# Optimization experiments

Measured on AMD Instinct MI355X. Metric: run time of the kernel, lower is better.

Reference implementation:

```python
import jax, jax.numpy as jnp
import numpy as np

B, S, F, P, D, H, L, FF, R = 64, 4096, 8, 16, 512, 8, 6, 2048, 8
NP = (S - P) // P + 1  # 256 patches (stride == patch_length)
DK = D // H
LORA_SCALING = 16.0 / 8.0  # lora_alpha / lora_rank


def setup_inputs() -> dict:
    key = jax.random.key(0)
    ks = iter(jax.random.split(key, 40))
    def nrm(shape, s=0.02):
        return jax.random.normal(next(ks), shape, jnp.float32) * s
    inp = {
        "x": jax.random.normal(next(ks), (B, S, F), jnp.float32),
        "patch_w": nrm((P * F, D)), "patch_b": jnp.zeros((D,), jnp.float32),
        "patch_ln_w": jnp.ones((D,), jnp.float32), "patch_ln_b": jnp.zeros((D,), jnp.float32),
        "pos_enc": nrm((1, NP, D)),
        "ln1_w": jnp.ones((L, D), jnp.float32), "ln1_b": jnp.zeros((L, D), jnp.float32),
        "q_w": nrm((L, D, D)), "q_b": jnp.zeros((L, D), jnp.float32),
        "k_w": nrm((L, D, D)), "k_b": jnp.zeros((L, D), jnp.float32),
        "v_w": nrm((L, D, D)), "v_b": jnp.zeros((L, D), jnp.float32),
        "lq_down": nrm((L, D, R)), "lq_up": nrm((L, R, D)),
        "lk_down": nrm((L, D, R)), "lk_up": nrm((L, R, D)),
        "lv_down": nrm((L, D, R)), "lv_up": nrm((L, R, D)),
        "o_w": nrm((L, D, D)), "o_b": jnp.zeros((L, D), jnp.float32),
        "ln2_w": jnp.ones((L, D), jnp.float32), "ln2_b": jnp.zeros((L, D), jnp.float32),
        "ff1_w": nrm((L, D, FF)), "ff1_b": jnp.zeros((L, FF), jnp.float32),
        "ff2_w": nrm((L, FF, D)), "ff2_b": jnp.zeros((L, D), jnp.float32),
        "norm_w": jnp.ones((D,), jnp.float32), "norm_b": jnp.zeros((D,), jnp.float32),
    }
    return inp


def _layer_norm(x, w, b):
    m = jnp.mean(x, -1, keepdims=True)
    v = jnp.mean(jnp.square(x - m), -1, keepdims=True)
    return (x - m) * jax.lax.rsqrt(v + 1e-5) * w + b


def _forward(x, patch_w, patch_b, patch_ln_w, patch_ln_b, pos_enc,
             ln1_w, ln1_b, q_w, q_b, k_w, k_b, v_w, v_b,
             lq_down, lq_up, lk_down, lk_up, lv_down, lv_up,
             o_w, o_b, ln2_w, ln2_b, ff1_w, ff1_b, ff2_w, ff2_b,
             norm_w, norm_b):
    # Patch embedding: [B,S,F] -> [B,F,S] -> unfold(stride==patch) -> [B,NP,F*P]
    patches = x.transpose(0, 2, 1).reshape(B, F, NP, P).transpose(0, 2, 1, 3).reshape(B, NP, F * P)
    h = _layer_norm(patches @ patch_w + patch_b, patch_ln_w, patch_ln_b) + pos_enc
    inv_scale = 1.0 / np.sqrt(DK).astype(np.float32)
    for i in range(L):
        y = _layer_norm(h, ln1_w[i], ln1_b[i])
        q = y @ q_w[i] + q_b[i] + (y @ lq_down[i]) @ lq_up[i] * LORA_SCALING
        k = y @ k_w[i] + k_b[i] + (y @ lk_down[i]) @ lk_up[i] * LORA_SCALING
        v = y @ v_w[i] + v_b[i] + (y @ lv_down[i]) @ lv_up[i] * LORA_SCALING
        q = q.reshape(B, NP, H, DK)
        k = k.reshape(B, NP, H, DK)
        v = v.reshape(B, NP, H, DK)
        scores = jnp.einsum('bqhd,bkhd->bhqk', q, k) * inv_scale
        probs = jax.nn.softmax(scores, axis=-1)
        attn = jnp.einsum('bhqk,bkhd->bqhd', probs, v).reshape(B, NP, D)
        h = h + attn @ o_w[i] + o_b[i]
        y = _layer_norm(h, ln2_w[i], ln2_b[i])
        ff = jax.nn.gelu(y @ ff1_w[i] + ff1_b[i], approximate=False) @ ff2_w[i] + ff2_b[i]
        h = h + ff
    h = _layer_norm(h, norm_w, norm_b)
    return h.mean(axis=1)  # [B, D]


def reference(x, patch_w, patch_b, patch_ln_w, patch_ln_b, pos_enc,
              ln1_w, ln1_b, q_w, q_b, k_w, k_b, v_w, v_b,
              lq_down, lq_up, lk_down, lk_up, lv_down, lv_up,
              o_w, o_b, ln2_w, ln2_b, ff1_w, ff1_b, ff2_w, ff2_b,
              norm_w, norm_b):
    return _forward(x, patch_w, patch_b, patch_ln_w, patch_ln_b, pos_enc,
                    ln1_w, ln1_b, q_w, q_b, k_w, k_b, v_w, v_b,
                    lq_down, lq_up, lk_down, lk_up, lv_down, lv_up,
                    o_w, o_b, ln2_w, ln2_b, ff1_w, ff1_b, ff2_w, ff2_b,
                    norm_w, norm_b)
```

## Files before the change

kernel.cpp:

```cpp
#include <hip/hip_runtime.h>
#include <cstdint>
#include <cstddef>

constexpr int BATCH = 64, SEQ = 4096, FEAT = 8, PLEN = 16;
constexpr int DMODEL = 512, NHEAD = 8, NLAYER = 6, DFF = 2048;
constexpr int NPATCH = 256, MROWS = BATCH * NPATCH;
constexpr int DK = 64;
constexpr int LDSP = 72;

typedef unsigned short u16t;
typedef __bf16 bf16t;
typedef bf16t bf16x8 __attribute__((ext_vector_type(8)));
typedef short s16x4 __attribute__((ext_vector_type(4)));
typedef float f32x4 __attribute__((ext_vector_type(4)));

__device__ __forceinline__ float b2f(u16t u) {
  union { unsigned int ui; float f; } v; v.ui = ((unsigned int)u) << 16; return v.f;
}
__device__ __forceinline__ u16t f2b(float f) {
  union { float f; unsigned int ui; } v; v.f = f;
  return (u16t)((v.ui + 0x7fffu + ((v.ui >> 16) & 1u)) >> 16);
}
__device__ __forceinline__ void g2l16(void* lds, const void* g) {
  __builtin_amdgcn_global_load_lds(
      (__attribute__((address_space(1))) void*)g,
      (__attribute__((address_space(3))) void*)lds, 16, 0, 0);
}

__device__ __forceinline__ float gelu_erf(float x) {
  const float z = fabsf(x) * 0.70710678118654752f;
  const float t = __builtin_amdgcn_rcpf(__builtin_fmaf(0.3275911f, z, 1.0f));
  float p = __builtin_fmaf(1.061405429f, t, -1.453152027f);
  p = __builtin_fmaf(p, t, 1.421413741f);
  p = __builtin_fmaf(p, t, -0.284496736f);
  p = __builtin_fmaf(p, t, 0.254829592f);
  const float e = __expf(-z * z);
  const float er = __builtin_fmaf(-p * t, e, 1.0f);
  const float s = copysignf(er, x);
  return 0.5f * x * (1.0f + s);
}

__global__ __launch_bounds__(256, 2) void k_gemm(
    const u16t* __restrict__ A, const u16t* __restrict__ Bt,
    const float* __restrict__ bias, const float* __restrict__ b2,
    const float* __restrict__ b3, float* __restrict__ Cf,
    u16t* __restrict__ Cb, int M, int N, int K, int mode)
{
  __shared__ __align__(16) u16t SH[3 * 12288];

  const int nbn = N >> 7;
  const int cpx = gridDim.x >> 3;
  const int wgid = (blockIdx.x & 7) * cpx + (blockIdx.x >> 3);
  const int bm = (wgid / nbn) << 8;
  const int bn = (wgid % nbn) << 7;

  const int tid = threadIdx.x, wave = tid >> 6, lane = tid & 63;
  const int lr = lane & 15, quad = lane >> 4;
  const int wm = (wave >> 1) << 7;
  const int wn = (wave & 1) << 6;

  const int srow = lane >> 2;
  const int sseg = (lane & 3) ^ ((lane >> 3) & 3);
  const u16t* gA = A + (size_t)(bm + wave * 64 + srow) * K + sseg * 8;
  const u16t* gB = Bt + (size_t)(bn + wave * 32 + srow) * K + sseg * 8;
  const size_t r16K = (size_t)16 * K;

  const int sw8 = (quad ^ ((lr >> 1) & 3)) << 3;
  const int aoff = (wm + lr) * 32 + sw8;
  const int boff = 8192 + (wn + lr) * 32 + sw8;

  f32x4 acc[4][8] = {};

  u16t* buf0 = SH;
  u16t* buf1 = SH + 12288;
  u16t* buf2 = SH + 24576;

  #pragma unroll
  for (int j = 0; j < 4; ++j) g2l16(&buf0[(wave * 4 + j) * 512], gA + (size_t)j * r16K);
  #pragma unroll
  for (int j = 0; j < 2; ++j) g2l16(&buf0[8192 + (wave * 2 + j) * 512], gB + (size_t)j * r16K);
  gA += 32; gB += 32;
  #pragma unroll
  for (int j = 0; j < 4; ++j) g2l16(&buf1[(wave * 4 + j) * 512], gA + (size_t)j * r16K);
  #pragma unroll
  for (int j = 0; j < 2; ++j) g2l16(&buf1[8192 + (wave * 2 + j) * 512], gB + (size_t)j * r16K);
  gA += 32; gB += 32;

  const int nt = K >> 5;
  for (int t = 0; t < nt - 1; ++t) {
    asm volatile("s_waitcnt vmcnt(6)" ::: "memory");
    __builtin_amdgcn_s_barrier();
    asm volatile("" ::: "memory");
    if (t + 2 < nt) {
      #pragma unroll
      for (int j = 0; j < 4; ++j) g2l16(&buf2[(wave * 4 + j) * 512], gA + (size_t)j * r16K);
      #pragma unroll
      for (int j = 0; j < 2; ++j) g2l16(&buf2[8192 + (wave * 2 + j) * 512], gB + (size_t)j * r16K);
      gA += 32; gB += 32;
    }
    bf16x8 af[8], bfr[4];
    #pragma unroll
    for (int i = 0; i < 8; ++i) af[i] = *(const bf16x8*)&buf0[aoff + i * 512];
    #pragma unroll
    for (int j = 0; j < 4; ++j) bfr[j] = *(const bf16x8*)&buf0[boff + j * 512];
    __builtin_amdgcn_s_setprio(1);
    #pragma unroll
    for (int j = 0; j < 4; ++j)
      #pragma unroll
      for (int i = 0; i < 8; ++i)
        acc[j][i] = __builtin_amdgcn_mfma_f32_16x16x32_bf16(bfr[j], af[i], acc[j][i], 0, 0, 0);
    __builtin_amdgcn_s_setprio(0);
    u16t* tmp = buf0; buf0 = buf1; buf1 = buf2; buf2 = tmp;
  }
  {
    asm volatile("s_waitcnt vmcnt(0)" ::: "memory");
    __builtin_amdgcn_s_barrier();
    asm volatile("" ::: "memory");
    bf16x8 af[8], bfr[4];
    #pragma unroll
    for (int i = 0; i < 8; ++i) af[i] = *(const bf16x8*)&buf0[aoff + i * 512];
    #pragma unroll
    for (int j = 0; j < 4; ++j) bfr[j] = *(const bf16x8*)&buf0[boff + j * 512];
    __builtin_amdgcn_s_setprio(1);
    #pragma unroll
    for (int j = 0; j < 4; ++j)
      #pragma unroll
      for (int i = 0; i < 8; ++i)
        acc[j][i] = __builtin_amdgcn_mfma_f32_16x16x32_bf16(bfr[j], af[i], acc[j][i], 0, 0, 0);
    __builtin_amdgcn_s_setprio(0);
  }

  const float* bp = bias;
  int reg0 = 0;
  if (bias && b2) { reg0 = (bn >> 9) << 9; bp = reg0 == 0 ? bias : (reg0 == 512 ? b2 : b3); }
  float4 bv[4];
  #pragma unroll
  for (int jN = 0; jN < 4; ++jN) {
    const int gn0 = bn + wn + jN * 16 + quad * 4;
    bv[jN] = bias ? *(const float4*)&bp[gn0 - reg0] : make_float4(0.f, 0.f, 0.f, 0.f);
  }

  if (mode <= 1) {
    __syncthreads();
    u16t* E = SH;
    #pragma unroll
    for (int jN = 0; jN < 4; ++jN) {
      const int cl = wn + jN * 16 + quad * 4;
      const int seg = cl >> 3, intra = cl & 7;
      #pragma unroll
      for (int iM = 0; iM < 8; ++iM) {
        const int r = wm + iM * 16 + lr;
        float v0 = acc[jN][iM][0] + bv[jN].x, v1 = acc[jN][iM][1] + bv[jN].y;
        float v2 = acc[jN][iM][2] + bv[jN].z, v3 = acc[jN][iM][3] + bv[jN].w;
        union { u16t h[4]; uint2 u; } pk;
        if (mode == 1) {
          pk.h[0] = f2b(gelu_erf(v0)); pk.h[1] = f2b(gelu_erf(v1));
          pk.h[2] = f2b(gelu_erf(v2)); pk.h[3] = f2b(gelu_erf(v3));
        } else {
          pk.h[0] = f2b(v0); pk.h[1] = f2b(v1); pk.h[2] = f2b(v2); pk.h[3] = f2b(v3);
        }
        *(uint2*)&E[r * 128 + ((seg ^ (r & 7)) << 3) + intra] = pk.u;
      }
    }
    __syncthreads();
    const int rr = tid >> 2, s0 = tid & 3;
    #pragma unroll
    for (int pass = 0; pass < 4; ++pass) {
      const int r = pass * 64 + rr;
      u16t* gout = Cb + (size_t)(bm + r) * N + bn;
      #pragma unroll
      for (int it = 0; it < 4; ++it) {
        const int s = s0 + it * 4;
        uint4 u = *(const uint4*)&E[r * 128 + ((s ^ (r & 7)) << 3)];
        *(uint4*)(gout + s * 8) = u;
      }
    }
  } else {
    #pragma unroll
    for (int jN = 0; jN < 4; ++jN) {
      const int gn0 = bn + wn + jN * 16 + quad * 4;
      #pragma unroll
      for (int iM = 0; iM < 8; ++iM) {
        const int gm = bm + wm + iM * 16 + lr;
        const size_t off = (size_t)gm * N + gn0;
        float v0 = acc[jN][iM][0] + bv[jN].x, v1 = acc[jN][iM][1] + bv[jN].y;
        float v2 = acc[jN][iM][2] + bv[jN].z, v3 = acc[jN][iM][3] + bv[jN].w;
        if (mode == 2) {
          float4 c = *(float4*)(Cf + off);
          c.x += v0; c.y += v1; c.z += v2; c.w += v3;
          *(float4*)(Cf + off) = c;
        } else {
          *(float4*)(Cf + off) = make_float4(v0, v1, v2, v3);
        }
      }
    }
  }
}

__global__ __launch_bounds__(256) void k_prep_w(
    const float* __restrict__ W, const float* __restrict__ down,
    const float* __restrict__ up, u16t* __restrict__ Wt, int K, int N,
    size_t ostride, int orow0)
{
  __shared__ float t[32][33];
  const int z = blockIdx.z;
  const float* Wz = W + (size_t)z * K * N;
  u16t* Wtz = Wt + (size_t)z * ostride + (size_t)orow0 * K;
  const int k0 = blockIdx.x * 32, n0 = blockIdx.y * 32;
  const int tx = threadIdx.x & 31, ty = threadIdx.x >> 5;
  for (int i = ty; i < 32; i += 8) {
    const int kk = k0 + i, nn = n0 + tx;
    float v = Wz[(size_t)kk * N + nn];
    if (down) {
      const float* dz = down + (size_t)z * K * 8 + (size_t)kk * 8;
      const float* uz = up + (size_t)z * 8 * N + nn;
      float lv = 0.f;
      #pragma unroll
      for (int r = 0; r < 8; ++r) lv += dz[r] * uz[(size_t)r * N];
      v += 2.0f * lv;
    }
    t[i][tx] = v;
  }
  __syncthreads();
  for (int i = ty; i < 32; i += 8)
    Wtz[(size_t)(n0 + i) * K + k0 + tx] = f2b(t[tx][i]);
}

__global__ void k_patch(const float* __restrict__ x, u16t* __restrict__ pt) {
  const int idx = blockIdx.x * 256 + threadIdx.x;
  const int col = idx & 127, row = idx >> 7;
  const int f = col >> 4, pp = col & 15;
  const int b = row >> 8, np = row & 255;
  pt[idx] = f2b(x[(((size_t)b << 12) + np * 16 + pp) * 8 + f]);
}

__global__ __launch_bounds__(256) void k_ln(
    const float* __restrict__ xin, const float* __restrict__ w,
    const float* __restrict__ bb, u16t* __restrict__ y)
{
  const int row = blockIdx.x * 4 + (threadIdx.x >> 6);
  const int lane = threadIdx.x & 63;
  const float4* xr = (const float4*)(xin + (size_t)row * 512);
  float4 a = xr[lane * 2], c = xr[lane * 2 + 1];
  float s = a.x + a.y + a.z + a.w + c.x + c.y + c.z + c.w;
  float qq = a.x * a.x + a.y * a.y + a.z * a.z + a.w * a.w +
             c.x * c.x + c.y * c.y + c.z * c.z + c.w * c.w;
  #pragma unroll
  for (int o = 32; o > 0; o >>= 1) { s += __shfl_xor(s, o); qq += __shfl_xor(qq, o); }
  const float mean = s * (1.f / 512.f);
  const float rs = rsqrtf(qq * (1.f / 512.f) - mean * mean + 1e-5f);
  const float4* wr = (const float4*)w; const float4* br = (const float4*)bb;
  float4 w0 = wr[lane * 2], w1 = wr[lane * 2 + 1];
  float4 b0 = br[lane * 2], b1 = br[lane * 2 + 1];
  union { u16t h[8]; uint4 v; } pk;
  pk.h[0] = f2b((a.x - mean) * rs * w0.x + b0.x);
  pk.h[1] = f2b((a.y - mean) * rs * w0.y + b0.y);
  pk.h[2] = f2b((a.z - mean) * rs * w0.z + b0.z);
  pk.h[3] = f2b((a.w - mean) * rs * w0.w + b0.w);
  pk.h[4] = f2b((c.x - mean) * rs * w1.x + b1.x);
  pk.h[5] = f2b((c.y - mean) * rs * w1.y + b1.y);
  pk.h[6] = f2b((c.z - mean) * rs * w1.z + b1.z);
  pk.h[7] = f2b((c.w - mean) * rs * w1.w + b1.w);
  *(uint4*)(y + (size_t)row * 512 + lane * 8) = pk.v;
}

__global__ __launch_bounds__(256) void k_ln_pos(
    const float* __restrict__ xin, const float* __restrict__ w,
    const float* __restrict__ bb, const float* __restrict__ pos,
    float* __restrict__ h)
{
  const int row = blockIdx.x * 4 + (threadIdx.x >> 6);
  const int lane = threadIdx.x & 63;
  const float4* xr = (const float4*)(xin + (size_t)row * 512);
  float4 a = xr[lane * 2], c = xr[lane * 2 + 1];
  float s = a.x + a.y + a.z + a.w + c.x + c.y + c.z + c.w;
  float qq = a.x * a.x + a.y * a.y + a.z * a.z + a.w * a.w +
             c.x * c.x + c.y * c.y + c.z * c.z + c.w * c.w;
  #pragma unroll
  for (int o = 32; o > 0; o >>= 1) { s += __shfl_xor(s, o); qq += __shfl_xor(qq, o); }
  const float mean = s * (1.f / 512.f);
  const float rs = rsqrtf(qq * (1.f / 512.f) - mean * mean + 1e-5f);
  const float4* wr = (const float4*)w; const float4* br = (const float4*)bb;
  float4 w0 = wr[lane * 2], w1 = wr[lane * 2 + 1];
  float4 b0 = br[lane * 2], b1 = br[lane * 2 + 1];
  const int np = row & 255;
  const float4* pr = (const float4*)(pos + (size_t)np * 512);
  float4 p0 = pr[lane * 2], p1 = pr[lane * 2 + 1];
  float4 o0, o1;
  o0.x = (a.x - mean) * rs * w0.x + b0.x + p0.x;
  o0.y = (a.y - mean) * rs * w0.y + b0.y + p0.y;
  o0.z = (a.z - mean) * rs * w0.z + b0.z + p0.z;
  o0.w = (a.w - mean) * rs * w0.w + b0.w + p0.w;
  o1.x = (c.x - mean) * rs * w1.x + b1.x + p1.x;
  o1.y = (c.y - mean) * rs * w1.y + b1.y + p1.y;
  o1.z = (c.z - mean) * rs * w1.z + b1.z + p1.z;
  o1.w = (c.w - mean) * rs * w1.w + b1.w + p1.w;
  float4* hr = (float4*)(h + (size_t)row * 512);
  hr[lane * 2] = o0; hr[lane * 2 + 1] = o1;
}

__global__ __launch_bounds__(256) void k_attn(
    const u16t* __restrict__ qkv, u16t* __restrict__ out)
{
  __shared__ __align__(16) u16t Qs[128 * LDSP];
  __shared__ __align__(16) u16t Ks[64 * LDSP];
  __shared__ __align__(16) u16t Vts[64 * LDSP];

  const int bh = blockIdx.x >> 1, half = blockIdx.x & 1;
  const int b = bh >> 3, hd = bh & 7;
  const int tid = threadIdx.x, wave = tid >> 6, lane = tid & 63;
  const int lr = lane & 15, quad = lane >> 4;

  const size_t rowbase = (size_t)b * 256;
  const u16t* qg = qkv + (rowbase + half * 128) * 1536 + hd * 64;
  const u16t* kg = qkv + rowbase * 1536 + 512 + hd * 64;
  const u16t* vg = qkv + rowbase * 1536 + 1024 + hd * 64;

  #pragma unroll
  for (int i = 0; i < 4; ++i) {
    const int idx = tid + i * 256, row = idx >> 3, seg = idx & 7;
    uint4 u = *(const uint4*)(qg + (size_t)row * 1536 + seg * 8);
    *(uint4*)&Qs[row * LDSP + seg * 8] = u;
  }
  __syncthreads();

  bf16x8 qf[2][2];
  #pragma unroll
  for (int qi = 0; qi < 2; ++qi)
    #pragma unroll
    for (int dh = 0; dh < 2; ++dh)
      qf[qi][dh] = *(const bf16x8*)&Qs[(wave * 32 + qi * 16 + lr) * LDSP + dh * 32 + quad * 8];

  f32x4 O[2][4] = {};
  float mrun[2] = {-1e30f, -1e30f}, lrun[2] = {0.f, 0.f};

  for (int c = 0; c < 4; ++c) {
    __syncthreads();
    #pragma unroll
    for (int i = 0; i < 2; ++i) {
      const int idx = tid + i * 256, row = idx >> 3, seg = idx & 7;
      uint4 u = *(const uint4*)(kg + (size_t)(c * 64 + row) * 1536 + seg * 8);
      *(uint4*)&Ks[row * LDSP + seg * 8] = u;
    }
    {
      const int key = tid & 63, dg = (tid >> 6) * 16;
      const u16t* vrow = vg + (size_t)(c * 64 + key) * 1536 + dg;
      union { u16t h[16]; uint4 v[2]; } tmp;
      tmp.v[0] = *(const uint4*)(vrow);
      tmp.v[1] = *(const uint4*)(vrow + 8);
      #pragma unroll
      for (int i = 0; i < 16; ++i)
        Vts[(dg + i) * LDSP + key] = tmp.h[i];
    }
    __syncthreads();

    #pragma unroll
    for (int qi = 0; qi < 2; ++qi) {
      f32x4 s[4];
      #pragma unroll
      for (int kt = 0; kt < 4; ++kt) {
        f32x4 a = {};
        #pragma unroll
        for (int dh = 0; dh < 2; ++dh) {
          bf16x8 kf = *(const bf16x8*)&Ks[(kt * 16 + lr) * LDSP + dh * 32 + quad * 8];
          a = __builtin_amdgcn_mfma_f32_16x16x32_bf16(kf, qf[qi][dh], a, 0, 0, 0);
        }
        s[kt] = a;
      }
      constexpr float SC = 0.125f * 1.44269504088896f;
      float cmax = -1e30f;
      #pragma unroll
      for (int kt = 0; kt < 4; ++kt)
        #pragma unroll
        for (int r = 0; r < 4; ++r) { s[kt][r] *= SC; cmax = fmaxf(cmax, s[kt][r]); }
      cmax = fmaxf(cmax, __shfl_xor(cmax, 16));
      cmax = fmaxf(cmax, __shfl_xor(cmax, 32));
      const float mn = fmaxf(mrun[qi], cmax);
      const float alpha = exp2f(mrun[qi] - mn);
      mrun[qi] = mn;
      float lsum = 0.f;
      s16x4 pf[4];
      #pragma unroll
      for (int kt = 0; kt < 4; ++kt) {
        #pragma unroll
        for (int r = 0; r < 4; ++r) {
          const u16t eb = f2b(exp2f(s[kt][r] - mn));
          pf[kt][r] = (short)eb;
          lsum += b2f(eb);
        }
      }
      lsum += __shfl_xor(lsum, 16);
      lsum += __shfl_xor(lsum, 32);
      lrun[qi] = lrun[qi] * alpha + lsum;
      #pragma unroll
      for (int dt = 0; dt < 4; ++dt) {
        f32x4 o = O[qi][dt];
        o[0] *= alpha; o[1] *= alpha; o[2] *= alpha; o[3] *= alpha;
        #pragma unroll
        for (int kt = 0; kt < 4; ++kt) {
          s16x4 vf = *(const s16x4*)&Vts[(dt * 16 + lr) * LDSP + kt * 16 + quad * 4];
          o = __builtin_amdgcn_mfma_f32_16x16x16bf16_1k(vf, pf[kt], o, 0, 0, 0);
        }
        O[qi][dt] = o;
      }
    }
  }
  #pragma unroll
  for (int qi = 0; qi < 2; ++qi) {
    const float rl = 1.f / lrun[qi];
    u16t* orow = out + (rowbase + half * 128 + wave * 32 + qi * 16 + lr) * 512 + hd * 64 + quad * 4;
    #pragma unroll
    for (int dt = 0; dt < 4; ++dt) {
      union { u16t h[4]; uint2 v; } pk;
      #pragma unroll
      for (int r = 0; r < 4; ++r) pk.h[r] = f2b(O[qi][dt][r] * rl);
      *(uint2*)(orow + dt * 16) = pk.v;
    }
  }
}

__global__ void k_mean(const u16t* __restrict__ y, float* __restrict__ out) {
  const int b = blockIdx.x, d = threadIdx.x;
  float s = 0.f;
  #pragma unroll 8
  for (int np = 0; np < 256; ++np) s += b2f(y[((size_t)b * 256 + np) * 512 + d]);
  out[(size_t)b * 512 + d] = s * (1.f / 256.f);
}

extern "C" void kernel_launch(void* const* d_in, const int* in_sizes, int n_in,
                              void* d_out, int out_size, void* d_ws, size_t ws_size,
                              hipStream_t stream)
{
  (void)in_sizes; (void)n_in; (void)out_size;
  const float* x        = (const float*)d_in[0];
  const float* patch_w  = (const float*)d_in[1];
  const float* patch_b  = (const float*)d_in[2];
  const float* patch_ln_w = (const float*)d_in[3];
  const float* patch_ln_b = (const float*)d_in[4];
  const float* pos_enc  = (const float*)d_in[5];
  const float* ln1_w    = (const float*)d_in[6];
  const float* ln1_b    = (const float*)d_in[7];
  const float* q_w      = (const float*)d_in[8];
  const float* q_b      = (const float*)d_in[9];
  const float* k_w      = (const float*)d_in[10];
  const float* k_b      = (const float*)d_in[11];
  const float* v_w      = (const float*)d_in[12];
  const float* v_b      = (const float*)d_in[13];
  const float* lq_down  = (const float*)d_in[14];
  const float* lq_up    = (const float*)d_in[15];
  const float* lk_down  = (const float*)d_in[16];
  const float* lk_up    = (const float*)d_in[17];
  const float* lv_down  = (const float*)d_in[18];
  const float* lv_up    = (const float*)d_in[19];
  const float* o_w      = (const float*)d_in[20];
  const float* o_b      = (const float*)d_in[21];
  const float* ln2_w    = (const float*)d_in[22];
  const float* ln2_b    = (const float*)d_in[23];
  const float* ff1_w    = (const float*)d_in[24];
  const float* ff1_b    = (const float*)d_in[25];
  const float* ff2_w    = (const float*)d_in[26];
  const float* ff2_b    = (const float*)d_in[27];
  const float* norm_w   = (const float*)d_in[28];
  const float* norm_b   = (const float*)d_in[29];
  float* out = (float*)d_out;

  char* p = (char*)d_ws;
  float* h  = (float*)p;  p += (size_t)MROWS * 512 * 4;
  u16t*  y  = (u16t*)p;   p += (size_t)MROWS * 512 * 2;
  char* uni = p;          p += (size_t)4 * MROWS * 512 * 2;
  u16t* qkvb = (u16t*)uni;
  u16t* ab = (u16t*)(uni + (size_t)MROWS * 1536 * 2);
  u16t* g  = (u16t*)uni;
  float* pe = (float*)uni;
  u16t* pt = (u16t*)(uni + (size_t)MROWS * 512 * 4);
  u16t* wqkv = (u16t*)p; p += (size_t)NLAYER * 1536 * 512 * 2;
  u16t* wo = (u16t*)p; p += (size_t)NLAYER * 512 * 512 * 2;
  u16t* w1 = (u16t*)p; p += (size_t)NLAYER * 512 * 2048 * 2;
  u16t* w2 = (u16t*)p; p += (size_t)NLAYER * 2048 * 512 * 2;
  u16t* wp = (u16t*)p; p += (size_t)512 * 128 * 2;
  if ((size_t)(p - (char*)d_ws) > ws_size) return;

  const dim3 blk(256);
  const size_t QKVS = (size_t)1536 * 512;
  k_prep_w<<<dim3(16, 16, NLAYER), blk, 0, stream>>>(q_w, lq_down, lq_up, wqkv, 512, 512, QKVS, 0);
  k_prep_w<<<dim3(16, 16, NLAYER), blk, 0, stream>>>(k_w, lk_down, lk_up, wqkv, 512, 512, QKVS, 512);
  k_prep_w<<<dim3(16, 16, NLAYER), blk, 0, stream>>>(v_w, lv_down, lv_up, wqkv, 512, 512, QKVS, 1024);
  k_prep_w<<<dim3(16, 16, NLAYER), blk, 0, stream>>>(o_w, nullptr, nullptr, wo, 512, 512, (size_t)512 * 512, 0);
  k_prep_w<<<dim3(16, 64, NLAYER), blk, 0, stream>>>(ff1_w, nullptr, nullptr, w1, 512, 2048, (size_t)512 * 2048, 0);
  k_prep_w<<<dim3(64, 16, NLAYER), blk, 0, stream>>>(ff2_w, nullptr, nullptr, w2, 2048, 512, (size_t)2048 * 512, 0);
  k_prep_w<<<dim3(4, 16, 1),       blk, 0, stream>>>(patch_w, nullptr, nullptr, wp, 128, 512, 0, 0);

  k_patch<<<dim3(MROWS * 128 / 256), blk, 0, stream>>>(x, pt);
  k_gemm<<<dim3(64 * 4), blk, 0, stream>>>(pt, wp, patch_b, nullptr, nullptr, pe, nullptr, MROWS, 512, 128, 3);
  k_ln_pos<<<dim3(MROWS / 4), blk, 0, stream>>>(pe, patch_ln_w, patch_ln_b, pos_enc, h);

  for (int i = 0; i < NLAYER; ++i) {
    const size_t ws512 = (size_t)i * 512 * 512, wsff = (size_t)i * 512 * 2048;
    k_ln<<<dim3(MROWS / 4), blk, 0, stream>>>(h, ln1_w + i * 512, ln1_b + i * 512, y);
    k_gemm<<<dim3(64 * 12), blk, 0, stream>>>(y, wqkv + i * QKVS, q_b + i * 512, k_b + i * 512,
                                              v_b + i * 512, nullptr, qkvb, MROWS, 1536, 512, 0);
    k_attn<<<dim3(1024), blk, 0, stream>>>(qkvb, ab);
    k_gemm<<<dim3(64 * 4), blk, 0, stream>>>(ab, wo + ws512, o_b + i * 512, nullptr, nullptr, h, nullptr, MROWS, 512, 512, 2);
    k_ln<<<dim3(MROWS / 4), blk, 0, stream>>>(h, ln2_w + i * 512, ln2_b + i * 512, y);
    k_gemm<<<dim3(64 * 16), blk, 0, stream>>>(y, w1 + wsff, ff1_b + i * 2048, nullptr, nullptr, nullptr, g, MROWS, 2048, 512, 1);
    k_gemm<<<dim3(64 * 4), blk, 0, stream>>>(g, w2 + wsff, ff2_b + i * 512, nullptr, nullptr, h, nullptr, MROWS, 512, 2048, 2);
  }
  k_ln<<<dim3(MROWS / 4), blk, 0, stream>>>(h, norm_w, norm_b, y);
  k_mean<<<dim3(BATCH), dim3(512), 0, stream>>>(y, out);
}
```

Before: 1.501 ms.

## Add 256x256-tile 512-thread GEMM kernel for QKV and FF1 projections

Adds a new GEMM kernel with 256x256 output tiles, 8 waves, K-step 64 with double-buffered LDS staging, and fine-grained phases that interleave global-to-LDS loads with MFMA sub-blocks. It is used for the QKV and FF1 projections, which have bf16 outputs. The larger tile raises arithmetic intensity and cuts redundant global loads of A and B. It also changes the staging address pattern in the existing GEMM so that consecutive waves load interleaved 16-row chunks. The cost is 128 KB of LDS per block and fewer blocks in flight, so a poor schedule could leave MFMA units idle.

After: 1.600 ms. 1.07x slower.

```diff
diff --git a/kernel.cpp b/kernel.cpp
--- a/kernel.cpp
+++ b/kernel.cpp
@@ -59,11 +59,9 @@
   const int wm = (wave >> 1) << 7;
   const int wn = (wave & 1) << 6;
 
-  const int srow = lane >> 2;
   const int sseg = (lane & 3) ^ ((lane >> 3) & 3);
-  const u16t* gA = A + (size_t)(bm + wave * 64 + srow) * K + sseg * 8;
-  const u16t* gB = Bt + (size_t)(bn + wave * 32 + srow) * K + sseg * 8;
-  const size_t r16K = (size_t)16 * K;
+  const u16t* gA = A + (size_t)(bm + (lane >> 2)) * K + sseg * 8;
+  const u16t* gB = Bt + (size_t)(bn + (lane >> 2)) * K + sseg * 8;
 
   const int sw8 = (quad ^ ((lr >> 1) & 3)) << 3;
   const int aoff = (wm + lr) * 32 + sw8;
@@ -75,29 +73,24 @@
   u16t* buf1 = SH + 12288;
   u16t* buf2 = SH + 24576;
 
-  #pragma unroll
-  for (int j = 0; j < 4; ++j) g2l16(&buf0[(wave * 4 + j) * 512], gA + (size_t)j * r16K);
-  #pragma unroll
-  for (int j = 0; j < 2; ++j) g2l16(&buf0[8192 + (wave * 2 + j) * 512], gB + (size_t)j * r16K);
-  gA += 32; gB += 32;
-  #pragma unroll
-  for (int j = 0; j < 4; ++j) g2l16(&buf1[(wave * 4 + j) * 512], gA + (size_t)j * r16K);
-  #pragma unroll
-  for (int j = 0; j < 2; ++j) g2l16(&buf1[8192 + (wave * 2 + j) * 512], gB + (size_t)j * r16K);
-  gA += 32; gB += 32;
+#define STAGE_R10(BUF_, S_) do {                                               \
+    g2l16((BUF_) + wave * 512,        gA + (size_t)(wave * 16) * K + (S_) * 32);   \
+    g2l16((BUF_) + (wave + 4) * 512,  gA + (size_t)((wave + 4) * 16) * K + (S_) * 32); \
+    g2l16((BUF_) + (wave + 8) * 512,  gA + (size_t)((wave + 8) * 16) * K + (S_) * 32); \
+    g2l16((BUF_) + (wave + 12) * 512, gA + (size_t)((wave + 12) * 16) * K + (S_) * 32); \
+    g2l16((BUF_) + 8192 + wave * 512, gB + (size_t)(wave * 16) * K + (S_) * 32);   \
+    g2l16((BUF_) + 8192 + (wave + 4) * 512, gB + (size_t)((wave + 4) * 16) * K + (S_) * 32); \
+  } while (0)
 
   const int nt = K >> 5;
+  STAGE_R10(buf0, 0);
+  STAGE_R10(buf1, 1);
+
   for (int t = 0; t < nt - 1; ++t) {
     asm volatile("s_waitcnt vmcnt(6)" ::: "memory");
     __builtin_amdgcn_s_barrier();
     asm volatile("" ::: "memory");
-    if (t + 2 < nt) {
-      #pragma unroll
-      for (int j = 0; j < 4; ++j) g2l16(&buf2[(wave * 4 + j) * 512], gA + (size_t)j * r16K);
-      #pragma unroll
-      for (int j = 0; j < 2; ++j) g2l16(&buf2[8192 + (wave * 2 + j) * 512], gB + (size_t)j * r16K);
-      gA += 32; gB += 32;
-    }
+    if (t + 2 < nt) STAGE_R10(buf2, t + 2);
     bf16x8 af[8], bfr[4];
     #pragma unroll
     for (int i = 0; i < 8; ++i) af[i] = *(const bf16x8*)&buf0[aoff + i * 512];
@@ -129,6 +122,7 @@
         acc[j][i] = __builtin_amdgcn_mfma_f32_16x16x32_bf16(bfr[j], af[i], acc[j][i], 0, 0, 0);
     __builtin_amdgcn_s_setprio(0);
   }
+#undef STAGE_R10
 
   const float* bp = bias;
   int reg0 = 0;
@@ -194,6 +188,152 @@
         }
       }
     }
+  }
+}
+
+__global__ __launch_bounds__(512, 2) void k_gemm256(
+    const u16t* __restrict__ A, const u16t* __restrict__ Bt,
+    const float* __restrict__ bias, const float* __restrict__ b2,
+    const float* __restrict__ b3, u16t* __restrict__ Cb,
+    int M, int N, int K, int mode)
+{
+  __shared__ __align__(16) u16t SH[65536];
+
+  const int nbn = N >> 8;
+  const int cpx = gridDim.x >> 3;
+  const int wgid = (blockIdx.x & 7) * cpx + (blockIdx.x >> 3);
+  const int bm = (wgid / nbn) << 8;
+  const int bn = (wgid % nbn) << 8;
+
+  const int tid = threadIdx.x, wave = tid >> 6, lane = tid & 63;
+  const int lr = lane & 15, quad = lane >> 4, lr7 = lane & 7;
+  const int wm = (wave >> 2) << 7;
+  const int wn = (wave & 3) << 6;
+  const int hA = wave >> 2;
+  const int hB = (wave >> 1) & 1;
+  const int rB0 = (wave & 1) << 6;
+
+  const int srow = tid >> 3;
+  const int sdst = srow * 64 + (tid & 7) * 8;
+  const int ssegx = ((tid & 7) ^ (srow & 7)) * 8;
+  const u16t* gA0 = A + (size_t)(bm + srow) * K + ssegx;
+  const u16t* gB0 = Bt + (size_t)(bn + srow) * K + ssegx;
+
+  f32x4 acc[4][8] = {};
+  bf16x8 af_[4][2], bfr_[2][2];
+  const int NT = K >> 6, NIT = NT >> 1;
+
+#define STG(T_, H_) do { if ((T_) < NT) {                                      \
+    const int dd_ = ((T_) & 1) * 2;                                            \
+    u16t* dst_; const u16t* sp_;                                               \
+    if ((H_) < 2) {                                                            \
+      dst_ = SH + (dd_ + (H_)) * 8192 + sdst;                                  \
+      sp_ = gA0 + (size_t)((H_) * 128) * K + (T_) * 64;                        \
+    } else {                                                                   \
+      dst_ = SH + 32768 + (dd_ + (H_) - 2) * 8192 + sdst;                      \
+      sp_ = gB0 + (size_t)(((H_) - 2) * 128) * K + (T_) * 64;                  \
+    }                                                                          \
+    g2l16(dst_, sp_); g2l16(dst_ + 4096, sp_ + (size_t)64 * K);                \
+  } } while (0)
+
+#define GATE2 asm volatile("s_waitcnt vmcnt(2)" ::: "memory")
+#define GATE0 asm volatile("s_waitcnt vmcnt(0)" ::: "memory")
+#define GNONE (void)0
+
+#define PHASE(D_, MQ_, NQ_, ST_, SHF_, GATE_) do {                             \
+    if ((NQ_) == 0) {                                                          \
+      _Pragma("unroll") for (int i = 0; i < 4; ++i)                            \
+        _Pragma("unroll") for (int kk = 0; kk < 2; ++kk)                       \
+          af_[i][kk] = *(const bf16x8*)&SH[((D_) * 2 + hA) * 8192 +            \
+              (((MQ_) * 4 + i) * 16 + lr) * 64 + (((kk * 4 + quad) ^ lr7) << 3)]; \
+    }                                                                          \
+    _Pragma("unroll") for (int j = 0; j < 2; ++j)                              \
+      _Pragma("unroll") for (int kk = 0; kk < 2; ++kk)                         \
+        bfr_[j][kk] = *(const bf16x8*)&SH[32768 + ((D_) * 2 + hB) * 8192 +     \
+            (rB0 + ((NQ_) * 2 + j) * 16 + lr) * 64 + (((kk * 4 + quad) ^ lr7) << 3)]; \
+    STG(ST_, SHF_);                                                            \
+    if ((NQ_) == 0) asm volatile("s_waitcnt lgkmcnt(8)" ::: "memory");         \
+    __builtin_amdgcn_s_barrier();                                              \
+    asm volatile("s_waitcnt lgkmcnt(0)" ::: "memory");                         \
+    __builtin_amdgcn_sched_barrier(0);                                         \
+    __builtin_amdgcn_s_setprio(1);                                             \
+    _Pragma("unroll") for (int j = 0; j < 2; ++j)                              \
+      _Pragma("unroll") for (int i = 0; i < 4; ++i)                            \
+        _Pragma("unroll") for (int kk = 0; kk < 2; ++kk)                       \
+          acc[(NQ_) * 2 + j][(MQ_) * 4 + i] = __builtin_amdgcn_mfma_f32_16x16x32_bf16( \
+              bfr_[j][kk], af_[i][kk], acc[(NQ_) * 2 + j][(MQ_) * 4 + i], 0, 0, 0); \
+    __builtin_amdgcn_s_setprio(0);                                             \
+    GATE_;                                                                     \
+    __builtin_amdgcn_s_barrier();                                              \
+  } while (0)
+
+  STG(0, 0); STG(0, 1); STG(0, 2); STG(0, 3); STG(1, 0);
+  GATE2;
+  __builtin_amdgcn_s_barrier();
+
+  for (int i = 0; i < NIT - 1; ++i) {
+    const int tb = 2 * i;
+    PHASE(0, 0, 0, tb + 1, 1, GNONE);
+    PHASE(0, 0, 1, tb + 1, 2, GNONE);
+    PHASE(0, 1, 0, tb + 1, 3, GNONE);
+    PHASE(0, 1, 1, tb + 2, 0, GATE2);
+    PHASE(1, 0, 0, tb + 2, 1, GNONE);
+    PHASE(1, 0, 1, tb + 2, 2, GNONE);
+    PHASE(1, 1, 0, tb + 2, 3, GNONE);
+    PHASE(1, 1, 1, tb + 3, 0, GATE2);
+  }
+  {
+    const int tb = 2 * (NIT - 1);
+    PHASE(0, 0, 0, tb + 1, 1, GNONE);
+    PHASE(0, 0, 1, tb + 1, 2, GNONE);
+    PHASE(0, 1, 0, tb + 1, 3, GNONE);
+    PHASE(0, 1, 1, tb + 2, 0, GATE0);
+    PHASE(1, 0, 0, tb + 2, 1, GNONE);
+    PHASE(1, 0, 1, tb + 2, 2, GNONE);
+    PHASE(1, 1, 0, tb + 2, 3, GNONE);
+    PHASE(1, 1, 1, tb + 3, 0, GATE0);
+  }
+#undef PHASE
+#undef STG
+
+  const float* bp = bias;
+  int reg0 = 0;
+  if (bias && b2) { reg0 = (bn >> 9) << 9; bp = reg0 == 0 ? bias : (reg0 == 512 ? b2 : b3); }
+  float4 bv[4];
+  #pragma unroll
+  for (int jN = 0; jN < 4; ++jN) {
+    const int gn0 = bn + wn + jN * 16 + quad * 4;
+    bv[jN] = bias ? *(const float4*)&bp[gn0 - reg0] : make_float4(0.f, 0.f, 0.f, 0.f);
+  }
+
+  u16t* E = SH;
+  #pragma unroll
+  for (int jN = 0; jN < 4; ++jN) {
+    const int cl = wn + jN * 16 + quad * 4;
+    const int seg = cl >> 3, intra = cl & 7;
+    #pragma unroll
+    for (int iM = 0; iM < 8; ++iM) {
+      const int r = wm + iM * 16 + lr;
+      float v0 = acc[jN][iM][0] + bv[jN].x, v1 = acc[jN][iM][1] + bv[jN].y;
+      float v2 = acc[jN][iM][2] + bv[jN].z, v3 = acc[jN][iM][3] + bv[jN].w;
+      union { u16t h[4]; uint2 u; } pk;
+      if (mode == 1) {
+        pk.h[0] = f2b(gelu_erf(v0)); pk.h[1] = f2b(gelu_erf(v1));
+        pk.h[2] = f2b(gelu_erf(v2)); pk.h[3] = f2b(gelu_erf(v3));
+      } else {
+        pk.h[0] = f2b(v0); pk.h[1] = f2b(v1); pk.h[2] = f2b(v2); pk.h[3] = f2b(v3);
+      }
+      *(uint2*)&E[r * 256 + ((seg ^ (r & 7)) << 3) + intra] = pk.u;
+    }
+  }
+  __syncthreads();
+  const int rr = tid >> 5, t32 = tid & 31;
+  const int seg16 = t32;
+  #pragma unroll
+  for (int pass = 0; pass < 16; ++pass) {
+    const int r = pass * 16 + rr;
+    uint4 u = *(const uint4*)&E[r * 256 + ((seg16 ^ (r & 7)) << 3)];
+    *(uint4*)(Cb + (size_t)(bm + r) * N + bn + seg16 * 8) = u;
   }
 }
 
@@ -481,6 +621,7 @@
   if ((size_t)(p - (char*)d_ws) > ws_size) return;
 
   const dim3 blk(256);
+  const dim3 gblk(512);
   const size_t QKVS = (size_t)1536 * 512;
   k_prep_w<<<dim3(16, 16, NLAYER), blk, 0, stream>>>(q_w, lq_down, lq_up, wqkv, 512, 512, QKVS, 0);
   k_prep_w<<<dim3(16, 16, NLAYER), blk, 0, stream>>>(k_w, lk_down, lk_up, wqkv, 512, 512, QKVS, 512);
@@ -497,12 +638,13 @@
   for (int i = 0; i < NLAYER; ++i) {
     const size_t ws512 = (size_t)i * 512 * 512, wsff = (size_t)i * 512 * 2048;
     k_ln<<<dim3(MROWS / 4), blk, 0, stream>>>(h, ln1_w + i * 512, ln1_b + i * 512, y);
-    k_gemm<<<dim3(64 * 12), blk, 0, stream>>>(y, wqkv + i * QKVS, q_b + i * 512, k_b + i * 512,
-                                              v_b + i * 512, nullptr, qkvb, MROWS, 1536, 512, 0);
+    k_gemm256<<<dim3(64 * 6), gblk, 0, stream>>>(y, wqkv + i * QKVS, q_b + i * 512, k_b + i * 512,
+                                                 v_b + i * 512, qkvb, MROWS, 1536, 512, 0);
     k_attn<<<dim3(1024), blk, 0, stream>>>(qkvb, ab);
     k_gemm<<<dim3(64 * 4), blk, 0, stream>>>(ab, wo + ws512, o_b + i * 512, nullptr, nullptr, h, nullptr, MROWS, 512, 512, 2);
     k_ln<<<dim3(MROWS / 4), blk, 0, stream>>>(h, ln2_w + i * 512, ln2_b + i * 512, y);
-    k_gemm<<<dim3(64 * 16), blk, 0, stream>>>(y, w1 + wsff, ff1_b + i * 2048, nullptr, nullptr, nullptr, g, MROWS, 2048, 512, 1);
+    k_gemm256<<<dim3(64 * 8), gblk, 0, stream>>>(y, w1 + wsff, ff1_b + i * 2048, nullptr, nullptr,
+                                                 g, MROWS, 2048, 512, 1);
     k_gemm<<<dim3(64 * 4), blk, 0, stream>>>(g, w2 + wsff, ff2_b + i * 512, nullptr, nullptr, h, nullptr, MROWS, 512, 2048, 2);
   }
   k_ln<<<dim3(MROWS / 4), blk, 0, stream>>>(h, norm_w, norm_b, y);
```
